# Performance work log

Measured on AMD Instinct MI355X. Metric: run time of the kernel, lower is better.

Reference implementation:

```python
import jax, jax.numpy as jnp
import numpy as np

B = 128
E, IN, H, OUT, ZD = 6, 1664, 512, 618, 32


def setup_inputs() -> dict:
    key = jax.random.key(0)
    ks = jax.random.split(key, 9)
    scale = 0.05
    return {
        "p_prev": jax.random.normal(ks[0], (B, IN), dtype=jnp.float32),
        "blending_coef": jax.random.uniform(ks[1], (B, E), dtype=jnp.float32),
        "z": jax.random.normal(ks[2], (B, ZD), dtype=jnp.float32),
        "w_l1": jax.random.normal(ks[3], (E, IN, H), dtype=jnp.float32) * scale,
        "b_l1": jax.random.normal(ks[4], (E, H), dtype=jnp.float32) * scale,
        "w_l2": jax.random.normal(ks[5], (E, H + ZD, H), dtype=jnp.float32) * scale,
        "b_l2": jax.random.normal(ks[6], (E, H + ZD, H)[0:0] + (E, H), dtype=jnp.float32) * scale,
        "w_l3": jax.random.normal(ks[7], (E, H + ZD, OUT), dtype=jnp.float32) * scale,
        "b_l3": jax.random.normal(ks[8], (E, OUT), dtype=jnp.float32) * scale,
    }


def _moe_layer(x, coef, w, b, use_act=True):
    # Per-sample blended weight matmul, fused as a single contraction:
    # y[b,o] = sum_i x[b,i] * (sum_e coef[b,e] * w[e,i,o]) + sum_e coef[b,e] * b[e,o]
    y = jnp.einsum("bi,eio,be->bo", x, w, coef) + jnp.einsum("be,eo->bo", coef, b)
    return jax.nn.elu(y) if use_act else y


def reference(p_prev, blending_coef, z, w_l1, b_l1, w_l2, b_l2, w_l3, b_l3):
    x = _moe_layer(p_prev, blending_coef, w_l1, b_l1)              # [B, H]
    x = _moe_layer(jnp.concatenate([x, z], axis=-1), blending_coef, w_l2, b_l2)  # [B, H]
    x = _moe_layer(jnp.concatenate([x, z], axis=-1), blending_coef, w_l3, b_l3, use_act=False)  # [B, OUT]
    return x
```

## Files before the change

### kernel.cpp

```cpp
#include <hip/hip_runtime.h>
#include <hip/hip_bf16.h>
#include <math.h>

#define B 128
#define E 6
#define IN_DIM 1664
#define H_DIM 512
#define OUT_DIM 618
#define ZD 32
#define K2 544

typedef __attribute__((ext_vector_type(8))) short short8;
typedef __attribute__((ext_vector_type(4))) float f32x4;
union U128 { uint4 u4; short8 s8; ushort us[8]; };

__device__ __forceinline__ uint pk2(float a, float b) {
    union { __hip_bfloat162 h2; uint u; } cv;
    cv.h2.x = __float2bfloat16(a);
    cv.h2.y = __float2bfloat16(b);
    return cv.u;
}
__device__ __forceinline__ float elu1(float x) { return x < 0.f ? expm1f(x) : x; }


__global__ __launch_bounds__(256) void init_y1(
    const float* __restrict__ coef, const float* __restrict__ b1,
    float* __restrict__ y1)
{
    const int t = blockIdx.x * 256 + threadIdx.x;
    const int b = t >> 7, o = (t & 127) << 2;
    float4 v = {0.f, 0.f, 0.f, 0.f};
    #pragma unroll
    for (int e = 0; e < E; ++e) {
        const float c = coef[b * E + e];
        const float4 bb = *reinterpret_cast<const float4*>(b1 + e * H_DIM + o);
        v.x = fmaf(c, bb.x, v.x); v.y = fmaf(c, bb.y, v.y);
        v.z = fmaf(c, bb.z, v.z); v.w = fmaf(c, bb.w, v.w);
    }
    *reinterpret_cast<float4*>(y1 + b * H_DIM + o) = v;
}

__global__ __launch_bounds__(256) void gemm1(
    const float* __restrict__ x,
    const float* __restrict__ coef,
    const float* __restrict__ w,
    const float* __restrict__ b2, const float* __restrict__ b3,
    float* __restrict__ y1, float* __restrict__ y2, float* __restrict__ out)
{
    __shared__ ushort bs[24][64][8];
    const int tid = threadIdx.x;

    if (blockIdx.y == 0) {
        const int t = blockIdx.x * 256 + tid;
        {
            const int b = t >> 7, o = (t & 127) << 2;
            float4 v = {0.f, 0.f, 0.f, 0.f};
            #pragma unroll
            for (int e = 0; e < E; ++e) {
                const float c = coef[b * E + e];
                const float4 bb = *reinterpret_cast<const float4*>(b2 + e * H_DIM + o);
                v.x = fmaf(c, bb.x, v.x); v.y = fmaf(c, bb.y, v.y);
                v.z = fmaf(c, bb.z, v.z); v.w = fmaf(c, bb.w, v.w);
            }
            *reinterpret_cast<float4*>(y2 + b * H_DIM + o) = v;
        }
        for (int i = t; i < B * OUT_DIM; i += 64 * 256) {
            const int b = i / OUT_DIM, o = i - b * OUT_DIM;
            float v = 0.f;
            #pragma unroll
            for (int e = 0; e < E; ++e)
                v = fmaf(coef[b * E + e], b3[e * OUT_DIM + o], v);
            out[i] = v;
        }
        return;
    }

    const int kb0 = (blockIdx.y - 1) * 4;
    const int n0 = (blockIdx.x & 31) * 16, rowbase = (blockIdx.x >> 5) * 64;
    const int l = tid & 63, wv = tid >> 6;
    const int tn = tid & 15, tq = tid >> 4;
    const int lp = ((tq >> 2) << 4) | tn, j0 = (2 * tq) & 7;
    const int row = rowbase + wv * 16 + (l & 15);
    const int kq = l >> 4;

    float ce[E];
    #pragma unroll
    for (int e = 0; e < E; ++e) ce[e] = coef[row * E + e];

    float xv[4][8];
    #pragma unroll
    for (int kbi = 0; kbi < 4; ++kbi) {
        const float* p = x + (size_t)row * IN_DIM + (kb0 + kbi) * 32 + kq * 8;
        const float4 a = *reinterpret_cast<const float4*>(p);
        const float4 b = *reinterpret_cast<const float4*>(p + 4);
        xv[kbi][0] = a.x; xv[kbi][1] = a.y; xv[kbi][2] = a.z; xv[kbi][3] = a.w;
        xv[kbi][4] = b.x; xv[kbi][5] = b.y; xv[kbi][6] = b.z; xv[kbi][7] = b.w;
    }

    #pragma unroll
    for (int bb = 0; bb < 2; ++bb) {
        float wr[12][2];
        #pragma unroll
        for (int ss = 0; ss < 12; ++ss) {
            const int s = bb * 12 + ss;
            const int e = s % E, kb = kb0 + s / E;
            const float* src = w + ((size_t)e * IN_DIM + kb * 32 + 2 * tq) * H_DIM + n0 + tn;
            wr[ss][0] = src[0];
            wr[ss][1] = src[H_DIM];
        }
        #pragma unroll
        for (int ss = 0; ss < 12; ++ss)
            *reinterpret_cast<uint*>(&bs[bb * 12 + ss][lp][j0]) =
                pk2(wr[ss][0], wr[ss][1]);
    }
    __syncthreads();

    f32x4 acc = {0.f, 0.f, 0.f, 0.f};
    #pragma unroll
    for (int s = 0; s < 24; ++s) {
        const int e = s % E, kbi = s / E;
        U128 a, b0;
        uint* au = reinterpret_cast<uint*>(&a);
        au[0] = pk2(xv[kbi][0] * ce[e], xv[kbi][1] * ce[e]);
        au[1] = pk2(xv[kbi][2] * ce[e], xv[kbi][3] * ce[e]);
        au[2] = pk2(xv[kbi][4] * ce[e], xv[kbi][5] * ce[e]);
        au[3] = pk2(xv[kbi][6] * ce[e], xv[kbi][7] * ce[e]);
        b0.u4 = *reinterpret_cast<const uint4*>(&bs[s][l][0]);
        acc = __builtin_amdgcn_mfma_f32_16x16x32_bf16(a.s8, b0.s8, acc, 0, 0, 0);
    }

    const int colB = n0 + (l & 15);
    const int rowE = rowbase + wv * 16 + ((l >> 4) << 2);
    #pragma unroll
    for (int r = 0; r < 4; ++r)
        atomicAdd(&y1[(size_t)(rowE + r) * H_DIM + colB], acc[r]);
}

template<int KPB, bool ZS, int NW, bool GUARD>
__device__ __forceinline__ void gemm_mid_body(
    const float* __restrict__ yin,
    const float* __restrict__ coef,
    const float* __restrict__ z,
    const float* __restrict__ w,
    float* __restrict__ yout,
    int n0, int rowbase, int kb0, ushort (*bs)[64][8])
{
    constexpr int NS = E * KPB;
    const int tid = threadIdx.x;
    const int l = tid & 63, wv = tid >> 6;
    const int tn = tid & 15, tq = tid >> 4;
    const int lp = ((tq >> 2) << 4) | tn, j0 = (2 * tq) & 7;
    const int row = rowbase + wv * 16 + (l & 15);
    const int kq = l >> 4;
    const bool okS = !GUARD || (n0 + tn) < NW;

    float wr[NS][2];
    #pragma unroll
    for (int s = 0; s < NS; ++s) {
        const int e = s % E, kb = kb0 + s / E;
        const float* src = w + ((size_t)e * K2 + kb * 32 + 2 * tq) * NW + n0 + tn;
        wr[s][0] = okS ? src[0] : 0.f;
        wr[s][1] = okS ? src[NW] : 0.f;
    }

    float ce[E];
    #pragma unroll
    for (int e = 0; e < E; ++e) ce[e] = coef[row * E + e];

    float v[KPB * 8];
    if (ZS) {
        const float4 a = *reinterpret_cast<const float4*>(z + row * ZD + kq * 8);
        const float4 b = *reinterpret_cast<const float4*>(z + row * ZD + kq * 8 + 4);
        v[0] = a.x; v[1] = a.y; v[2] = a.z; v[3] = a.w;
        v[4] = b.x; v[5] = b.y; v[6] = b.z; v[7] = b.w;
    } else {
        #pragma unroll
        for (int kbi = 0; kbi < KPB; ++kbi) {
            const float* p = yin + (size_t)row * H_DIM + (kb0 + kbi) * 32 + kq * 8;
            const float4 a = *reinterpret_cast<const float4*>(p);
            const float4 b = *reinterpret_cast<const float4*>(p + 4);
            v[kbi*8+0] = elu1(a.x); v[kbi*8+1] = elu1(a.y);
            v[kbi*8+2] = elu1(a.z); v[kbi*8+3] = elu1(a.w);
            v[kbi*8+4] = elu1(b.x); v[kbi*8+5] = elu1(b.y);
            v[kbi*8+6] = elu1(b.z); v[kbi*8+7] = elu1(b.w);
        }
    }

    #pragma unroll
    for (int s = 0; s < NS; ++s)
        *reinterpret_cast<uint*>(&bs[s][lp][j0]) = pk2(wr[s][0], wr[s][1]);
    __syncthreads();

    f32x4 acc = {0.f, 0.f, 0.f, 0.f};
    #pragma unroll
    for (int s = 0; s < NS; ++s) {
        const int e = s % E, kbi = s / E;
        U128 a, b0;
        uint* au = reinterpret_cast<uint*>(&a);
        au[0] = pk2(v[kbi*8+0] * ce[e], v[kbi*8+1] * ce[e]);
        au[1] = pk2(v[kbi*8+2] * ce[e], v[kbi*8+3] * ce[e]);
        au[2] = pk2(v[kbi*8+4] * ce[e], v[kbi*8+5] * ce[e]);
        au[3] = pk2(v[kbi*8+6] * ce[e], v[kbi*8+7] * ce[e]);
        b0.u4 = *reinterpret_cast<const uint4*>(&bs[s][l][0]);
        acc = __builtin_amdgcn_mfma_f32_16x16x32_bf16(a.s8, b0.s8, acc, 0, 0, 0);
    }

    const int colB = n0 + (l & 15);
    const int rowE = rowbase + wv * 16 + ((l >> 4) << 2);
    if (!GUARD || colB < NW) {
        #pragma unroll
        for (int r = 0; r < 4; ++r)
            atomicAdd(&yout[(size_t)(rowE + r) * NW + colB], acc[r]);
    }
}

__global__ __launch_bounds__(256) void gemm_l2(
    const float* __restrict__ y1, const float* __restrict__ coef,
    const float* __restrict__ z, const float* __restrict__ w2,
    float* __restrict__ y2)
{
    __shared__ ushort bs[12][64][8];
    const int n0 = (blockIdx.x & 31) * 16, rowbase = (blockIdx.x >> 5) * 64;
    const int sp = blockIdx.y;
    if (sp < 8)
        gemm_mid_body<2, false, H_DIM, false>(y1, coef, z, w2, y2,
                                              n0, rowbase, sp * 2, bs);
    else
        gemm_mid_body<1, true, H_DIM, false>(y1, coef, z, w2, y2,
                                             n0, rowbase, 16, bs);
}

__global__ __launch_bounds__(256) void gemm_l3(
    const float* __restrict__ y2, const float* __restrict__ coef,
    const float* __restrict__ z, const float* __restrict__ w3,
    float* __restrict__ out)
{
    __shared__ ushort bs[12][64][8];
    const int nt = blockIdx.x % 40, rt = blockIdx.x / 40;
    const int n0 = nt * 16, rowbase = rt * 64;
    const int sp = blockIdx.y;
    if (sp < 8)
        gemm_mid_body<2, false, OUT_DIM, true>(y2, coef, z, w3, out,
                                               n0, rowbase, sp * 2, bs);
    else
        gemm_mid_body<1, true, OUT_DIM, true>(y2, coef, z, w3, out,
                                              n0, rowbase, 16, bs);
}

extern "C" void kernel_launch(void* const* d_in, const int* in_sizes, int n_in,
                              void* d_out, int out_size, void* d_ws, size_t ws_size,
                              hipStream_t stream)
{
    const float* p_prev = (const float*)d_in[0];
    const float* coef   = (const float*)d_in[1];
    const float* z      = (const float*)d_in[2];
    const float* w1     = (const float*)d_in[3];
    const float* b1     = (const float*)d_in[4];
    const float* w2     = (const float*)d_in[5];
    const float* b2     = (const float*)d_in[6];
    const float* w3     = (const float*)d_in[7];
    const float* b3     = (const float*)d_in[8];
    float* out = (float*)d_out;

    float* y1 = (float*)d_ws;
    float* y2 = y1 + (size_t)B * H_DIM;

    init_y1<<<64, 256, 0, stream>>>(coef, b1, y1);
    gemm1<<<dim3(64, 14), 256, 0, stream>>>(p_prev, coef, w1, b2, b3,
                                            y1, y2, out);
    gemm_l2<<<dim3(64, 9), 256, 0, stream>>>(y1, coef, z, w2, y2);
    gemm_l3<<<dim3(80, 9), 256, 0, stream>>>(y2, coef, z, w3, out);
}
```

Before: 44.87 us.

## Fuse four kernels into one persistent kernel with software grid barriers

Replaces the four separate launches (bias init and three MoE GEMM layers) with one persistent kernel of 256 blocks. The blocks loop over the former grid's jobs and use a hand-written global barrier built on atomic arrive/release flags in workspace. Intermediate activations are read with relaxed agent-scope atomic loads. The goal is to remove launch gaps between layers. In exchange it adds a memset launch and barrier spin costs, and it relies on all 256 blocks being co-resident with relaxed-ordering visibility.

```diff
diff --git a/kernel.cpp b/kernel.cpp
--- a/kernel.cpp
+++ b/kernel.cpp
@@ -1,5 +1,4 @@
 #include <hip/hip_runtime.h>
-#include <hip/hip_bf16.h>
 #include <math.h>
 
 #define B 128
@@ -9,74 +8,64 @@
 #define OUT_DIM 618
 #define ZD 32
 #define K2 544
+#define GRID 256
+#define NT 256
 
 typedef __attribute__((ext_vector_type(8))) short short8;
 typedef __attribute__((ext_vector_type(4))) float f32x4;
 union U128 { uint4 u4; short8 s8; ushort us[8]; };
 
+__device__ __forceinline__ ushort f2bf(float f) {
+    uint u = __float_as_uint(f);
+    u += 0x7fffu + ((u >> 16) & 1u);
+    return (ushort)(u >> 16);
+}
 __device__ __forceinline__ uint pk2(float a, float b) {
-    union { __hip_bfloat162 h2; uint u; } cv;
-    cv.h2.x = __float2bfloat16(a);
-    cv.h2.y = __float2bfloat16(b);
-    return cv.u;
+    return (uint)f2bf(a) | ((uint)f2bf(b) << 16);
 }
 __device__ __forceinline__ float elu1(float x) { return x < 0.f ? expm1f(x) : x; }
 
-
-__global__ __launch_bounds__(256) void init_y1(
-    const float* __restrict__ coef, const float* __restrict__ b1,
-    float* __restrict__ y1)
-{
-    const int t = blockIdx.x * 256 + threadIdx.x;
-    const int b = t >> 7, o = (t & 127) << 2;
-    float4 v = {0.f, 0.f, 0.f, 0.f};
-    #pragma unroll
-    for (int e = 0; e < E; ++e) {
-        const float c = coef[b * E + e];
-        const float4 bb = *reinterpret_cast<const float4*>(b1 + e * H_DIM + o);
-        v.x = fmaf(c, bb.x, v.x); v.y = fmaf(c, bb.y, v.y);
-        v.z = fmaf(c, bb.z, v.z); v.w = fmaf(c, bb.w, v.w);
-    }
-    *reinterpret_cast<float4*>(y1 + b * H_DIM + o) = v;
-}
-
-__global__ __launch_bounds__(256) void gemm1(
-    const float* __restrict__ x,
-    const float* __restrict__ coef,
-    const float* __restrict__ w,
-    const float* __restrict__ b2, const float* __restrict__ b3,
-    float* __restrict__ y1, float* __restrict__ y2, float* __restrict__ out)
-{
-    __shared__ ushort bs[24][64][8];
+__device__ __forceinline__ void ast(float* p, float v) {
+    __hip_atomic_store(p, v, __ATOMIC_RELAXED, __HIP_MEMORY_SCOPE_AGENT);
+}
+__device__ __forceinline__ float ald(const float* p) {
+    return __hip_atomic_load(p, __ATOMIC_RELAXED, __HIP_MEMORY_SCOPE_AGENT);
+}
+
+__device__ __forceinline__ void gbar(uint* arrive, uint* release, int i) {
+    __syncthreads();
+    if (blockIdx.x == 0) {
+        if (threadIdx.x > 0) {
+            while (__hip_atomic_load(&arrive[threadIdx.x * 16],
+                                     __ATOMIC_RELAXED,
+                                     __HIP_MEMORY_SCOPE_AGENT) < (uint)(i + 1))
+                __builtin_amdgcn_s_sleep(2);
+        }
+        __syncthreads();
+        if (threadIdx.x == 0)
+            __hip_atomic_store(&release[i * 16], 1u, __ATOMIC_RELAXED,
+                               __HIP_MEMORY_SCOPE_AGENT);
+    } else {
+        if (threadIdx.x == 0) {
+            __hip_atomic_store(&arrive[blockIdx.x * 16], (uint)(i + 1),
+                               __ATOMIC_RELAXED, __HIP_MEMORY_SCOPE_AGENT);
+            while (__hip_atomic_load(&release[i * 16], __ATOMIC_RELAXED,
+                                     __HIP_MEMORY_SCOPE_AGENT) == 0)
+                __builtin_amdgcn_s_sleep(2);
+        }
+        __syncthreads();
+    }
+}
+
+
+__device__ __forceinline__ void job_l1(
+    const float* __restrict__ x, const float* __restrict__ coef,
+    const float* __restrict__ w, float* __restrict__ y1,
+    int t, int sp, ushort (*bs)[64][8])
+{
     const int tid = threadIdx.x;
-
-    if (blockIdx.y == 0) {
-        const int t = blockIdx.x * 256 + tid;
-        {
-            const int b = t >> 7, o = (t & 127) << 2;
-            float4 v = {0.f, 0.f, 0.f, 0.f};
-            #pragma unroll
-            for (int e = 0; e < E; ++e) {
-                const float c = coef[b * E + e];
-                const float4 bb = *reinterpret_cast<const float4*>(b2 + e * H_DIM + o);
-                v.x = fmaf(c, bb.x, v.x); v.y = fmaf(c, bb.y, v.y);
-                v.z = fmaf(c, bb.z, v.z); v.w = fmaf(c, bb.w, v.w);
-            }
-            *reinterpret_cast<float4*>(y2 + b * H_DIM + o) = v;
-        }
-        for (int i = t; i < B * OUT_DIM; i += 64 * 256) {
-            const int b = i / OUT_DIM, o = i - b * OUT_DIM;
-            float v = 0.f;
-            #pragma unroll
-            for (int e = 0; e < E; ++e)
-                v = fmaf(coef[b * E + e], b3[e * OUT_DIM + o], v);
-            out[i] = v;
-        }
-        return;
-    }
-
-    const int kb0 = (blockIdx.y - 1) * 4;
-    const int n0 = (blockIdx.x & 31) * 16, rowbase = (blockIdx.x >> 5) * 64;
+    const int kb0 = sp * 4;
+    const int n0 = (t & 31) * 16, rowbase = (t >> 5) * 64;
     const int l = tid & 63, wv = tid >> 6;
     const int tn = tid & 15, tq = tid >> 4;
     const int lp = ((tq >> 2) << 4) | tn, j0 = (2 * tq) & 7;
@@ -97,6 +86,7 @@
         xv[kbi][4] = b.x; xv[kbi][5] = b.y; xv[kbi][6] = b.z; xv[kbi][7] = b.w;
     }
 
+    __syncthreads();
     #pragma unroll
     for (int bb = 0; bb < 2; ++bb) {
         float wr[12][2];
@@ -137,13 +127,11 @@
 }
 
 template<int KPB, bool ZS, int NW, bool GUARD>
-__device__ __forceinline__ void gemm_mid_body(
-    const float* __restrict__ yin,
-    const float* __restrict__ coef,
-    const float* __restrict__ z,
-    const float* __restrict__ w,
-    float* __restrict__ yout,
-    int n0, int rowbase, int kb0, ushort (*bs)[64][8])
+__device__ __forceinline__ void job_mid(
+    const float* __restrict__ yin, const float* __restrict__ coef,
+    const float* __restrict__ z, const float* __restrict__ w,
+    float* __restrict__ yout, int n0, int rowbase, int kb0,
+    ushort (*bs)[64][8])
 {
     constexpr int NS = E * KPB;
     const int tid = threadIdx.x;
@@ -177,15 +165,13 @@
         #pragma unroll
         for (int kbi = 0; kbi < KPB; ++kbi) {
             const float* p = yin + (size_t)row * H_DIM + (kb0 + kbi) * 32 + kq * 8;
-            const float4 a = *reinterpret_cast<const float4*>(p);
-            const float4 b = *reinterpret_cast<const float4*>(p + 4);
-            v[kbi*8+0] = elu1(a.x); v[kbi*8+1] = elu1(a.y);
-            v[kbi*8+2] = elu1(a.z); v[kbi*8+3] = elu1(a.w);
-            v[kbi*8+4] = elu1(b.x); v[kbi*8+5] = elu1(b.y);
-            v[kbi*8+6] = elu1(b.z); v[kbi*8+7] = elu1(b.w);
-        }
-    }
-
+            #pragma unroll
+            for (int j = 0; j < 8; ++j)
+                v[kbi * 8 + j] = elu1(ald(p + j));
+        }
+    }
+
+    __syncthreads();
     #pragma unroll
     for (int s = 0; s < NS; ++s)
         *reinterpret_cast<uint*>(&bs[s][lp][j0]) = pk2(wr[s][0], wr[s][1]);
@@ -214,37 +200,63 @@
     }
 }
 
-__global__ __launch_bounds__(256) void gemm_l2(
-    const float* __restrict__ y1, const float* __restrict__ coef,
-    const float* __restrict__ z, const float* __restrict__ w2,
-    float* __restrict__ y2)
-{
-    __shared__ ushort bs[12][64][8];
-    const int n0 = (blockIdx.x & 31) * 16, rowbase = (blockIdx.x >> 5) * 64;
-    const int sp = blockIdx.y;
-    if (sp < 8)
-        gemm_mid_body<2, false, H_DIM, false>(y1, coef, z, w2, y2,
-                                              n0, rowbase, sp * 2, bs);
-    else
-        gemm_mid_body<1, true, H_DIM, false>(y1, coef, z, w2, y2,
-                                             n0, rowbase, 16, bs);
-}
-
-__global__ __launch_bounds__(256) void gemm_l3(
-    const float* __restrict__ y2, const float* __restrict__ coef,
-    const float* __restrict__ z, const float* __restrict__ w3,
-    float* __restrict__ out)
-{
-    __shared__ ushort bs[12][64][8];
-    const int nt = blockIdx.x % 40, rt = blockIdx.x / 40;
-    const int n0 = nt * 16, rowbase = rt * 64;
-    const int sp = blockIdx.y;
-    if (sp < 8)
-        gemm_mid_body<2, false, OUT_DIM, true>(y2, coef, z, w3, out,
-                                               n0, rowbase, sp * 2, bs);
-    else
-        gemm_mid_body<1, true, OUT_DIM, true>(y2, coef, z, w3, out,
-                                              n0, rowbase, 16, bs);
+__global__ __launch_bounds__(NT) void moe_net(
+    const float* __restrict__ x, const float* __restrict__ coef,
+    const float* __restrict__ z,
+    const float* __restrict__ w1, const float* __restrict__ b1,
+    const float* __restrict__ w2, const float* __restrict__ b2,
+    const float* __restrict__ w3, const float* __restrict__ b3,
+    float* y1, float* y2, uint* arrive, uint* release, float* out)
+{
+    __shared__ ushort bs[24][64][8];
+    const int bid = blockIdx.x, tid = threadIdx.x;
+    const int gt = bid * NT + tid;
+
+    {
+        const int b = gt >> 9, o = gt & 511;
+        float v = 0.f;
+        #pragma unroll
+        for (int e = 0; e < E; ++e) v = fmaf(coef[b * E + e], b1[e * H_DIM + o], v);
+        ast(&y1[gt], v);
+    }
+    {
+        const int b = gt >> 9, o = gt & 511;
+        float v = 0.f;
+        #pragma unroll
+        for (int e = 0; e < E; ++e) v = fmaf(coef[b * E + e], b2[e * H_DIM + o], v);
+        ast(&y2[gt], v);
+    }
+    for (int i = gt; i < B * OUT_DIM; i += GRID * NT) {
+        const int b = i / OUT_DIM, o = i - b * OUT_DIM;
+        float v = 0.f;
+        #pragma unroll
+        for (int e = 0; e < E; ++e) v = fmaf(coef[b * E + e], b3[e * OUT_DIM + o], v);
+        ast(&out[i], v);
+    }
+    gbar(arrive, release, 0);
+
+    for (int job = bid; job < 832; job += GRID)
+        job_l1(x, coef, w1, y1, job & 63, job >> 6, bs);
+    gbar(arrive, release, 1);
+
+    for (int job = bid; job < 576; job += GRID) {
+        const int t = job & 63, sp = job >> 6;
+        const int n0 = (t & 31) * 16, rb = (t >> 5) * 64;
+        if (sp < 8)
+            job_mid<2, false, H_DIM, false>(y1, coef, z, w2, y2, n0, rb, sp * 2, bs);
+        else
+            job_mid<1, true, H_DIM, false>(y1, coef, z, w2, y2, n0, rb, 16, bs);
+    }
+    gbar(arrive, release, 2);
+
+    for (int job = bid; job < 720; job += GRID) {
+        const int t = job % 80, sp = job / 80;
+        const int n0 = (t % 40) * 16, rb = (t / 40) * 64;
+        if (sp < 8)
+            job_mid<2, false, OUT_DIM, true>(y2, coef, z, w3, out, n0, rb, sp * 2, bs);
+        else
+            job_mid<1, true, OUT_DIM, true>(y2, coef, z, w3, out, n0, rb, 16, bs);
+    }
 }
 
 extern "C" void kernel_launch(void* const* d_in, const int* in_sizes, int n_in,
@@ -262,12 +274,13 @@
     const float* b3     = (const float*)d_in[8];
     float* out = (float*)d_out;
 
-    float* y1 = (float*)d_ws;
-    float* y2 = y1 + (size_t)B * H_DIM;
-
-    init_y1<<<64, 256, 0, stream>>>(coef, b1, y1);
-    gemm1<<<dim3(64, 14), 256, 0, stream>>>(p_prev, coef, w1, b2, b3,
-                                            y1, y2, out);
-    gemm_l2<<<dim3(64, 9), 256, 0, stream>>>(y1, coef, z, w2, y2);
-    gemm_l3<<<dim3(80, 9), 256, 0, stream>>>(y2, coef, z, w3, out);
-}
+    char* p = (char*)d_ws;
+    uint* arrive  = (uint*)p; p += GRID * 64;
+    uint* release = (uint*)p; p += 16 * 64;
+    float* y1 = (float*)p;    p += (size_t)B * H_DIM * 4;
+    float* y2 = (float*)p;
+
+    hipMemsetAsync(arrive, 0, GRID * 64 + 16 * 64, stream);
+    moe_net<<<GRID, NT, 0, stream>>>(p_prev, coef, z, w1, b1, w2, b2, w3, b3,
+                                     y1, y2, arrive, release, out);
+}
```

After: 69.83 us. 1.56x slower.
